# Kernel tuning notes

Hardware: AMD Instinct MI355X
Metric: run time of the kernel (lower is better)

The kernel has to match this reference:

```python
import jax, jax.numpy as jnp
import numpy as np

N_HEADS = 16
DIMS = 1024
HEAD_SIZE = DIMS // N_HEADS


def setup_inputs() -> dict:
    key = jax.random.key(0)
    k1, k2, k3, k4, k5 = jax.random.split(key, 5)
    x = jax.random.normal(k1, (1, 4096, DIMS), dtype=jnp.float32)
    s = 1.0 / np.sqrt(DIMS)
    w_qkv = jax.random.uniform(k2, (3 * DIMS, DIMS), jnp.float32, -s, s)
    b_qkv = jax.random.uniform(k3, (3 * DIMS,), jnp.float32, -s, s)
    w_o = jax.random.uniform(k4, (DIMS, DIMS), jnp.float32, -s, s)
    b_o = jax.random.uniform(k5, (DIMS,), jnp.float32, -s, s)
    return {"x": x, "w_qkv": w_qkv, "b_qkv": b_qkv, "w_o": w_o, "b_o": b_o,
            "causal_mask": 1}


def reference(x, w_qkv, b_qkv, w_o, b_o, causal_mask):
    B, S, D = x.shape
    qkv = x @ w_qkv.T + b_qkv                      # [B,S,3D]
    q, k, v = jnp.split(qkv, 3, axis=-1)
    def heads(t):
        return t.reshape(B, S, N_HEADS, HEAD_SIZE).transpose(0, 2, 1, 3)  # [B,H,S,hd]
    q, k, v = heads(q), heads(k), heads(v)
    scores = jnp.einsum("bhsd,bhtd->bhst", q, k)   # [B,H,S,S]
    if causal_mask:
        tri = jnp.triu(jnp.ones((S, S), dtype=bool), k=1)
        scores = jnp.where(tri, -jnp.inf, scores)  # mask BEFORE scale, as in torch code
    scores = scores / np.sqrt(HEAD_SIZE)
    weights = jax.nn.softmax(scores, axis=-1)
    out = jnp.einsum("bhst,bhtd->bhsd", weights, v)  # [B,H,S,hd]
    out = out.transpose(0, 2, 1, 3).reshape(B, S, D)
    return out @ w_o.T + b_o
```

## Files before the change

### kernel.cpp

```cpp
#include <hip/hip_runtime.h>
#include <hip/hip_bf16.h>
#include <stdint.h>

typedef __attribute__((ext_vector_type(8))) short short8;
typedef __attribute__((ext_vector_type(4))) float f32x4;
typedef __attribute__((ext_vector_type(16))) float f32x16;
typedef __attribute__((ext_vector_type(2))) unsigned int uint2u;
typedef __hip_bfloat16 bf16;

#define S_LEN 4096
#define DMODEL 1024
#define NH 16
#define HD 64
#define QSCALE 0.1803368801111f

static __device__ inline uint2 pack4(float4 v) {
  union { uint2 u; bf16 h[4]; } p;
  p.h[0] = (bf16)v.x; p.h[1] = (bf16)v.y; p.h[2] = (bf16)v.z; p.h[3] = (bf16)v.w;
  return p.u;
}

static __device__ inline uint32_t pack2(float a, float b) {
  union { uint32_t u; bf16 h[2]; } p;
  p.h[0] = (bf16)a; p.h[1] = (bf16)b;
  return p.u;
}

static __device__ inline void gload_lds16(const bf16* g, bf16* l) {
  __builtin_amdgcn_global_load_lds(
      (const __attribute__((address_space(1))) unsigned int*)g,
      (__attribute__((address_space(3))) unsigned int*)l, 16, 0, 0);
}

static __device__ inline int rot_idx(int r, int c) {
  return r * 64 + ((c + ((r & 7) << 3)) & 63);
}

__global__ __launch_bounds__(256)
void cvt_all(const float* __restrict__ x, const float* __restrict__ wq,
             const float* __restrict__ wo, bf16* __restrict__ xb,
             bf16* __restrict__ wqb, bf16* __restrict__ wob) {
  const int nx = S_LEN * DMODEL;
  const int nq = 3 * DMODEL * DMODEL;
  const int no = DMODEL * DMODEL;
  int i = (blockIdx.x * 256 + threadIdx.x) * 4;
  if (i < nx) {
    *(uint2*)(xb + i) = pack4(*(const float4*)(x + i));
  } else if (i < nx + nq) {
    int j = i - nx;
    *(uint2*)(wqb + j) = pack4(*(const float4*)(wq + j));
  } else if (i < nx + nq + no) {
    int j = i - nx - nq;
    *(uint2*)(wob + j) = pack4(*(const float4*)(wo + j));
  }
}

__global__ __launch_bounds__(256)
void gemm_qkv(const bf16* __restrict__ A, const bf16* __restrict__ B,
              const float* __restrict__ bias, bf16* __restrict__ qkv2,
              bf16* __restrict__ vt) {
  const int K = DMODEL;
  __shared__ bf16 sA[128 * 64];
  __shared__ bf16 sB[128 * 64];
  const int tid  = threadIdx.x;
  const int lane = tid & 63;
  const int wave = tid >> 6;
  const int wm = wave >> 1, wn = wave & 1;
  const int tileM = blockIdx.y * 128;
  const int tileN = blockIdx.x * 128;

  const int lrow = lane & 15;
  const int quad = lane >> 4;
  const int kq   = quad * 8;

  f32x4 acc[4][4];
#pragma unroll
  for (int i = 0; i < 4; i++)
#pragma unroll
    for (int j = 0; j < 4; j++) acc[i][j] = (f32x4){0.f, 0.f, 0.f, 0.f};

  const int trl = lane >> 3;
  const int cgl = (((lane & 7) - trl) & 7) << 3;
  const bf16* aP[4];
  const bf16* bP[4];
#pragma unroll
  for (int c = 0; c < 4; c++) {
    int ch = wave * 4 + c;
    aP[c] = A + (size_t)(tileM + ch * 8 + trl) * K + cgl;
    bP[c] = B + (size_t)(tileN + ch * 8 + trl) * K + cgl;
  }

  for (int k0 = 0; k0 < K; k0 += 64) {
    __syncthreads();
#pragma unroll
    for (int c = 0; c < 4; c++) {
      int ch = wave * 4 + c;
      gload_lds16(aP[c] + k0, sA + ch * 512);
      gload_lds16(bP[c] + k0, sB + ch * 512);
    }
    __syncthreads();
#pragma unroll
    for (int ks = 0; ks < 2; ks++) {
      short8 afrag[4], bfrag[4];
#pragma unroll
      for (int mi = 0; mi < 4; mi++)
        afrag[mi] = *(const short8*)(sA + rot_idx(wm * 64 + mi * 16 + lrow, ks * 32 + kq));
#pragma unroll
      for (int ni = 0; ni < 4; ni++)
        bfrag[ni] = *(const short8*)(sB + rot_idx(wn * 64 + ni * 16 + lrow, ks * 32 + kq));
#pragma unroll
      for (int mi = 0; mi < 4; mi++)
#pragma unroll
        for (int ni = 0; ni < 4; ni++)
          acc[mi][ni] = __builtin_amdgcn_mfma_f32_16x16x32_bf16(afrag[mi], bfrag[ni], acc[mi][ni], 0, 0, 0);
    }
  }

#pragma unroll
  for (int ni = 0; ni < 4; ni++) {
    int col = tileN + wn * 64 + ni * 16 + lrow;
    float bv = bias[col];
    if (col < 2 * DMODEL) {
      float sc = (col < DMODEL) ? QSCALE : 1.0f;
#pragma unroll
      for (int mi = 0; mi < 4; mi++) {
        int row0 = tileM + wm * 64 + mi * 16 + quad * 4;
#pragma unroll
        for (int r = 0; r < 4; r++)
          qkv2[(size_t)(row0 + r) * 2048 + col] = (bf16)((acc[mi][ni][r] + bv) * sc);
      }
    } else {
      int cc = col - 2 * DMODEL;
      int hh = cc >> 6, dd = cc & 63;
      bf16* vrow = vt + ((size_t)(hh * 64 + dd)) * S_LEN;
#pragma unroll
      for (int mi = 0; mi < 4; mi++) {
        int row0 = tileM + wm * 64 + mi * 16 + quad * 4;
        float4 v = {acc[mi][ni][0] + bv, acc[mi][ni][1] + bv,
                    acc[mi][ni][2] + bv, acc[mi][ni][3] + bv};
        *(uint2*)(vrow + row0) = pack4(v);
      }
    }
  }
}

__global__ __launch_bounds__(256)
void gemm_oproj(const bf16* __restrict__ A, const bf16* __restrict__ B,
                const float* __restrict__ bias, float* __restrict__ C) {
  const int K = DMODEL, N = DMODEL;
  __shared__ bf16 sA[128 * 64];
  __shared__ bf16 sB[64 * 64];
  const int tid  = threadIdx.x;
  const int lane = tid & 63;
  const int wave = tid >> 6;
  const int wm = wave >> 1, wn = wave & 1;
  const int tileM = blockIdx.y * 128;
  const int tileN = blockIdx.x * 64;

  const int lrow = lane & 15;
  const int quad = lane >> 4;
  const int kq   = quad * 8;

  f32x4 acc[4][2];
#pragma unroll
  for (int i = 0; i < 4; i++)
#pragma unroll
    for (int j = 0; j < 2; j++) acc[i][j] = (f32x4){0.f, 0.f, 0.f, 0.f};

  const int trl = lane >> 3;
  const int cgl = (((lane & 7) - trl) & 7) << 3;
  const bf16* aP[4];
  const bf16* bP[2];
#pragma unroll
  for (int c = 0; c < 4; c++) {
    int ch = wave * 4 + c;
    aP[c] = A + (size_t)(tileM + ch * 8 + trl) * K + cgl;
  }
#pragma unroll
  for (int c = 0; c < 2; c++) {
    int ch = wave * 2 + c;
    bP[c] = B + (size_t)(tileN + ch * 8 + trl) * K + cgl;
  }

  for (int k0 = 0; k0 < K; k0 += 64) {
    __syncthreads();
#pragma unroll
    for (int c = 0; c < 4; c++)
      gload_lds16(aP[c] + k0, sA + (wave * 4 + c) * 512);
#pragma unroll
    for (int c = 0; c < 2; c++)
      gload_lds16(bP[c] + k0, sB + (wave * 2 + c) * 512);
    __syncthreads();
#pragma unroll
    for (int ks = 0; ks < 2; ks++) {
      short8 afrag[4], bfrag[2];
#pragma unroll
      for (int mi = 0; mi < 4; mi++)
        afrag[mi] = *(const short8*)(sA + rot_idx(wm * 64 + mi * 16 + lrow, ks * 32 + kq));
#pragma unroll
      for (int ni = 0; ni < 2; ni++)
        bfrag[ni] = *(const short8*)(sB + rot_idx(wn * 32 + ni * 16 + lrow, ks * 32 + kq));
#pragma unroll
      for (int mi = 0; mi < 4; mi++)
#pragma unroll
        for (int ni = 0; ni < 2; ni++)
          acc[mi][ni] = __builtin_amdgcn_mfma_f32_16x16x32_bf16(afrag[mi], bfrag[ni], acc[mi][ni], 0, 0, 0);
    }
  }

#pragma unroll
  for (int ni = 0; ni < 2; ni++) {
    int col = tileN + wn * 32 + ni * 16 + lrow;
    float bv = bias[col];
#pragma unroll
    for (int mi = 0; mi < 4; mi++) {
      int row0 = tileM + wm * 64 + mi * 16 + quad * 4;
#pragma unroll
      for (int r = 0; r < 4; r++)
        C[(size_t)(row0 + r) * N + col] = acc[mi][ni][r] + bv;
    }
  }
}

__global__ __launch_bounds__(256)
void gemm_qkv_f32(const float* __restrict__ A, const float* __restrict__ B,
                  const float* __restrict__ bias, bf16* __restrict__ qkv2,
                  bf16* __restrict__ vt) {
  const int K = DMODEL;
  __shared__ bf16 sA[128 * 64];
  __shared__ bf16 sB[128 * 64];
  const int tid  = threadIdx.x;
  const int lane = tid & 63;
  const int wave = tid >> 6;
  const int wm = wave >> 1, wn = wave & 1;
  const int tileM = blockIdx.y * 128;
  const int tileN = blockIdx.x * 128;
  const int lrow = lane & 15;
  const int quad = lane >> 4;
  const int kq   = quad * 8;

  f32x4 acc[4][4];
#pragma unroll
  for (int i = 0; i < 4; i++)
#pragma unroll
    for (int j = 0; j < 4; j++) acc[i][j] = (f32x4){0.f, 0.f, 0.f, 0.f};

  const int r0 = tid >> 4;
  const int cc = (tid & 15) * 4;

  for (int k0 = 0; k0 < K; k0 += 64) {
    uint2 ra[8], rb[8];
#pragma unroll
    for (int i = 0; i < 8; i++) {
      int row = r0 + i * 16;
      ra[i] = pack4(*(const float4*)(A + (size_t)(tileM + row) * K + k0 + cc));
      rb[i] = pack4(*(const float4*)(B + (size_t)(tileN + row) * K + k0 + cc));
    }
    __syncthreads();
#pragma unroll
    for (int i = 0; i < 8; i++) {
      int row = r0 + i * 16;
      *(uint2*)(sA + row * 64 + cc) = ra[i];
      *(uint2*)(sB + row * 64 + cc) = rb[i];
    }
    __syncthreads();
#pragma unroll
    for (int ks = 0; ks < 2; ks++) {
      short8 afrag[4], bfrag[4];
#pragma unroll
      for (int mi = 0; mi < 4; mi++)
        afrag[mi] = *(const short8*)(sA + (wm * 64 + mi * 16 + lrow) * 64 + ks * 32 + kq);
#pragma unroll
      for (int ni = 0; ni < 4; ni++)
        bfrag[ni] = *(const short8*)(sB + (wn * 64 + ni * 16 + lrow) * 64 + ks * 32 + kq);
#pragma unroll
      for (int mi = 0; mi < 4; mi++)
#pragma unroll
        for (int ni = 0; ni < 4; ni++)
          acc[mi][ni] = __builtin_amdgcn_mfma_f32_16x16x32_bf16(afrag[mi], bfrag[ni], acc[mi][ni], 0, 0, 0);
    }
  }
#pragma unroll
  for (int ni = 0; ni < 4; ni++) {
    int col = tileN + wn * 64 + ni * 16 + lrow;
    float bv = bias[col];
    if (col < 2 * DMODEL) {
      float sc = (col < DMODEL) ? QSCALE : 1.0f;
#pragma unroll
      for (int mi = 0; mi < 4; mi++) {
        int row0 = tileM + wm * 64 + mi * 16 + quad * 4;
#pragma unroll
        for (int r = 0; r < 4; r++)
          qkv2[(size_t)(row0 + r) * 2048 + col] = (bf16)((acc[mi][ni][r] + bv) * sc);
      }
    } else {
      int c2 = col - 2 * DMODEL;
      int hh = c2 >> 6, dd = c2 & 63;
      bf16* vrow = vt + ((size_t)(hh * 64 + dd)) * S_LEN;
#pragma unroll
      for (int mi = 0; mi < 4; mi++) {
        int row0 = tileM + wm * 64 + mi * 16 + quad * 4;
        float4 v = {acc[mi][ni][0] + bv, acc[mi][ni][1] + bv,
                    acc[mi][ni][2] + bv, acc[mi][ni][3] + bv};
        *(uint2*)(vrow + row0) = pack4(v);
      }
    }
  }
}

__global__ __launch_bounds__(256)
void gemm_oproj_f32w(const bf16* __restrict__ A, const float* __restrict__ B,
                     const float* __restrict__ bias, float* __restrict__ C) {
  const int K = DMODEL, N = DMODEL;
  __shared__ bf16 sA[128 * 64];
  __shared__ bf16 sB[128 * 64];
  const int tid  = threadIdx.x;
  const int lane = tid & 63;
  const int wave = tid >> 6;
  const int wm = wave >> 1, wn = wave & 1;
  const int tileM = blockIdx.y * 128;
  const int tileN = blockIdx.x * 128;
  const int lrow = lane & 15;
  const int quad = lane >> 4;
  const int kq   = quad * 8;

  f32x4 acc[4][4];
#pragma unroll
  for (int i = 0; i < 4; i++)
#pragma unroll
    for (int j = 0; j < 4; j++) acc[i][j] = (f32x4){0.f, 0.f, 0.f, 0.f};

  const int a_r0 = tid >> 3;
  const int a_cc = (tid & 7) * 8;
  const int b_r0 = tid >> 4;
  const int b_cc = (tid & 15) * 4;

  for (int k0 = 0; k0 < K; k0 += 64) {
    uint4 ra[4];
    uint2 rb[8];
#pragma unroll
    for (int i = 0; i < 4; i++)
      ra[i] = *(const uint4*)(A + (size_t)(tileM + a_r0 + i * 32) * K + k0 + a_cc);
#pragma unroll
    for (int i = 0; i < 8; i++)
      rb[i] = pack4(*(const float4*)(B + (size_t)(tileN + b_r0 + i * 16) * K + k0 + b_cc));
    __syncthreads();
#pragma unroll
    for (int i = 0; i < 4; i++)
      *(uint4*)(sA + (a_r0 + i * 32) * 64 + a_cc) = ra[i];
#pragma unroll
    for (int i = 0; i < 8; i++)
      *(uint2*)(sB + (b_r0 + i * 16) * 64 + b_cc) = rb[i];
    __syncthreads();
#pragma unroll
    for (int ks = 0; ks < 2; ks++) {
      short8 afrag[4], bfrag[4];
#pragma unroll
      for (int mi = 0; mi < 4; mi++)
        afrag[mi] = *(const short8*)(sA + (wm * 64 + mi * 16 + lrow) * 64 + ks * 32 + kq);
#pragma unroll
      for (int ni = 0; ni < 4; ni++)
        bfrag[ni] = *(const short8*)(sB + (wn * 64 + ni * 16 + lrow) * 64 + ks * 32 + kq);
#pragma unroll
      for (int mi = 0; mi < 4; mi++)
#pragma unroll
        for (int ni = 0; ni < 4; ni++)
          acc[mi][ni] = __builtin_amdgcn_mfma_f32_16x16x32_bf16(afrag[mi], bfrag[ni], acc[mi][ni], 0, 0, 0);
    }
  }
#pragma unroll
  for (int ni = 0; ni < 4; ni++) {
    int col = tileN + wn * 64 + ni * 16 + lrow;
    float bv = bias[col];
#pragma unroll
    for (int mi = 0; mi < 4; mi++) {
      int row0 = tileM + wm * 64 + mi * 16 + quad * 4;
#pragma unroll
      for (int r = 0; r < 4; r++)
        C[(size_t)(row0 + r) * N + col] = acc[mi][ni][r] + bv;
    }
  }
}

__global__ __launch_bounds__(256, 4)
void attn_kernel(const bf16* __restrict__ qkv2, const bf16* __restrict__ vt,
                 bf16* __restrict__ attn_out, const int* __restrict__ causal_ptr) {
  __shared__ bf16 sQ[64 * 64];
  __shared__ bf16 sK[2][64 * 64];
  __shared__ bf16 sV[2][64 * 64];

  const int tid  = threadIdx.x;
  const int lane = tid & 63;
  const int wave = tid >> 6;
  const int qh   = wave >> 1;
  const int kh   = wave & 1;

  const int id  = blockIdx.y * 64 + blockIdx.x;
  const int xcd = id & 7;
  const int jj  = id >> 3;
  const int hh  = jj >> 6;
  const int h   = xcd + (hh << 3);
  const int qw  = jj & 63;
  const int qi  = hh ? (63 - qw) : qw;
  const int qbase = qi * 64;
  const bool causal = (*causal_ptr) != 0;

  const int l31 = lane & 31;
  const int hi  = lane >> 5;

  const int trl = lane >> 3;
  const int cgl = (((lane & 7) - trl) & 7) << 3;

  const bf16* Qb = qkv2 + h * HD;
  const bf16* Kb = qkv2 + DMODEL + h * HD;
  const bf16* Vb = vt + (size_t)(h * HD) * S_LEN;

#pragma unroll
  for (int i = 0; i < 2; i++) {
    int ch = wave * 2 + i;
    gload_lds16(Qb + (size_t)(qbase + ch * 8 + trl) * 2048 + cgl, sQ + ch * 512);
  }
#pragma unroll
  for (int i = 0; i < 2; i++) {
    int ch = wave * 2 + i;
    int trow = ch * 8 + trl;
    gload_lds16(Kb + (size_t)trow * 2048 + cgl, sK[0] + ch * 512);
    gload_lds16(Vb + (size_t)trow * S_LEN + cgl, sV[0] + ch * 512);
  }

  f32x16 oacc[2];
#pragma unroll
  for (int nc = 0; nc < 2; nc++)
#pragma unroll
    for (int e = 0; e < 16; e++) oacc[nc][e] = 0.f;
  float l_st = 0.f;

  const int nkt = causal ? (qi + 1) : (S_LEN / 64);
  const int wrmin = qbase + qh * 32;
  const int wrmax = wrmin + 31;
  const int q_g   = wrmin + l31;

  __syncthreads();
  short8 qf[4];
#pragma unroll
  for (int kd = 0; kd < 4; kd++)
    qf[kd] = *(const short8*)(sQ + rot_idx(qh * 32 + l31, kd * 16 + hi * 8));

  for (int jt = 0; jt < nkt; jt++) {
    const int cur = jt & 1;
    const int kbase = jt * 64;
    __syncthreads();

    if (jt + 1 < nkt) {
      const int kb2 = kbase + 64;
#pragma unroll
      for (int i = 0; i < 2; i++) {
        int ch = wave * 2 + i;
        int trow = ch * 8 + trl;
        gload_lds16(Kb + (size_t)(kb2 + trow) * 2048 + cgl, sK[cur ^ 1] + ch * 512);
        gload_lds16(Vb + (size_t)trow * S_LEN + kb2 + cgl, sV[cur ^ 1] + ch * 512);
      }
    }
    const int kh32 = kbase + kh * 32;
    if (causal && kh32 > wrmax) continue;

    uint32_t pw[2][4];
    {
      f32x16 sacc;
#pragma unroll
      for (int e = 0; e < 16; e++) sacc[e] = 0.f;
      __builtin_amdgcn_s_setprio(1);
#pragma unroll
      for (int kd = 0; kd < 4; kd++) {
        short8 kf = *(const short8*)(sK[cur] + rot_idx(kh * 32 + l31, kd * 16 + hi * 8));
        sacc = __builtin_amdgcn_mfma_f32_32x32x16_bf16(kf, qf[kd], sacc, 0, 0, 0);
      }
      __builtin_amdgcn_s_setprio(0);
      const bool nm = causal && (kh32 + 31 > wrmin);
      float p[16];
      float psum = 0.f;
#pragma unroll
      for (int g = 0; g < 4; g++) {
#pragma unroll
        for (int r = 0; r < 4; r++) {
          float v = __builtin_amdgcn_exp2f(sacc[g * 4 + r]);
          if (nm) {
            int kg = kh32 + g * 8 + hi * 4 + r;
            if (kg > q_g) v = 0.f;
          }
          p[g * 4 + r] = v;
          psum += v;
        }
      }
      l_st += psum;
      uint32_t pku[4][2];
#pragma unroll
      for (int g = 0; g < 4; g++) {
#pragma unroll
        for (int h2 = 0; h2 < 2; h2++)
          pku[g][h2] = pack2(p[g * 4 + h2 * 2], p[g * 4 + h2 * 2 + 1]);
      }
#pragma unroll
      for (int c2 = 0; c2 < 2; c2++) {
#pragma unroll
        for (int h2 = 0; h2 < 2; h2++) {
          uint2u sw = __builtin_amdgcn_permlane32_swap(
              pku[2 * c2][h2], pku[2 * c2 + 1][h2], false, false);
          pw[c2][h2]     = sw[0];
          pw[c2][2 + h2] = sw[1];
        }
      }
    }

    __builtin_amdgcn_s_setprio(1);
#pragma unroll
    for (int c2 = 0; c2 < 2; c2++) {
      if (causal && (kh32 + c2 * 16 > wrmax)) continue;
      union { short8 s; uint32_t u[4]; } pf;
#pragma unroll
      for (int w = 0; w < 4; w++) pf.u[w] = pw[c2][w];
#pragma unroll
      for (int nc = 0; nc < 2; nc++) {
        short8 vf = *(const short8*)(sV[cur] +
            rot_idx(nc * 32 + l31, (kh * 2 + c2) * 16 + hi * 8));
        oacc[nc] = __builtin_amdgcn_mfma_f32_32x32x16_bf16(pf.s, vf, oacc[nc], 0, 0, 0);
      }
    }
    __builtin_amdgcn_s_setprio(0);
  }

  __syncthreads();
  float ltot = l_st + __shfl_xor(l_st, 32);
  float* obuf = (float*)sK;
  float* lbuf = (float*)sV;
  if (kh == 1) {
    float* ob = obuf + qh * 2048;
#pragma unroll
    for (int nc = 0; nc < 2; nc++)
#pragma unroll
      for (int e = 0; e < 16; e++)
        ob[(nc * 16 + e) * 64 + lane] = oacc[nc][e];
    if (hi == 0) lbuf[qh * 32 + l31] = ltot;
  }
  __syncthreads();
  if (kh == 0) {
    float* ob = obuf + qh * 2048;
#pragma unroll
    for (int nc = 0; nc < 2; nc++)
#pragma unroll
      for (int e = 0; e < 16; e++)
        oacc[nc][e] += ob[(nc * 16 + e) * 64 + lane];
    ltot += lbuf[qh * 32 + l31];
    if (hi == 0) lbuf[64 + qh * 32 + l31] = ltot;
    float invl[4][4];
#pragma unroll
    for (int g = 0; g < 4; g++) {
      f32x4 lv = *(const f32x4*)(lbuf + 64 + qh * 32 + g * 8 + hi * 4);
#pragma unroll
      for (int r = 0; r < 4; r++) invl[g][r] = 1.0f / fmaxf(lv[r], 1e-30f);
    }
#pragma unroll
    for (int nc = 0; nc < 2; nc++) {
#pragma unroll
      for (int g = 0; g < 4; g++) {
#pragma unroll
        for (int r = 0; r < 4; r++) {
          int qg = qbase + qh * 32 + g * 8 + hi * 4 + r;
          int col = h * HD + nc * 32 + l31;
          attn_out[(size_t)qg * DMODEL + col] = (bf16)(oacc[nc][g * 4 + r] * invl[g][r]);
        }
      }
    }
  }
}

extern "C" void kernel_launch(void* const* d_in, const int* in_sizes, int n_in,
                              void* d_out, int out_size, void* d_ws, size_t ws_size,
                              hipStream_t stream) {
  const float* x     = (const float*)d_in[0];
  const float* w_qkv = (const float*)d_in[1];
  const float* b_qkv = (const float*)d_in[2];
  const float* w_o   = (const float*)d_in[3];
  const float* b_o   = (const float*)d_in[4];
  const int*   cm    = (const int*)d_in[5];

  char* ws = (char*)d_ws;
  bf16* qkv2 = (bf16*)ws;
  bf16* vt   = (bf16*)(ws + 16777216);
  bf16* attn = (bf16*)(ws + 25165824);
  bf16* xb   = (bf16*)(ws + 33554432);
  bf16* wqb  = (bf16*)(ws + 41943040);
  bf16* wob  = (bf16*)(ws + 48234496);

  dim3 blk(256);
  const bool fast = (ws_size >= (size_t)50331648);

  if (fast) {
    const int ntot = S_LEN * DMODEL + 3 * DMODEL * DMODEL + DMODEL * DMODEL;
    cvt_all<<<dim3((ntot / 4 + 255) / 256), blk, 0, stream>>>(
        x, w_qkv, w_o, xb, wqb, wob);
    gemm_qkv<<<dim3(3 * DMODEL / 128, S_LEN / 128), blk, 0, stream>>>(
        xb, wqb, b_qkv, qkv2, vt);
    attn_kernel<<<dim3(S_LEN / 64, NH), blk, 0, stream>>>(qkv2, vt, attn, cm);
    gemm_oproj<<<dim3(DMODEL / 64, S_LEN / 128), blk, 0, stream>>>(
        attn, wob, b_o, (float*)d_out);
  } else {
    gemm_qkv_f32<<<dim3(3 * DMODEL / 128, S_LEN / 128), blk, 0, stream>>>(
        x, w_qkv, b_qkv, qkv2, vt);
    attn_kernel<<<dim3(S_LEN / 64, NH), blk, 0, stream>>>(qkv2, vt, attn, cm);
    gemm_oproj_f32w<<<dim3(DMODEL / 128, S_LEN / 128), blk, 0, stream>>>(
        attn, w_o, b_o, (float*)d_out);
  }
}
```

Before: 221.0 us.

## Shrink attention LDS to two tiles to double occupancy

```diff
diff --git a/kernel.cpp b/kernel.cpp
--- a/kernel.cpp
+++ b/kernel.cpp
@@ -382,12 +382,11 @@
   }
 }
 
-__global__ __launch_bounds__(256, 4)
+__global__ __launch_bounds__(256, 8)
 void attn_kernel(const bf16* __restrict__ qkv2, const bf16* __restrict__ vt,
                  bf16* __restrict__ attn_out, const int* __restrict__ causal_ptr) {
-  __shared__ bf16 sQ[64 * 64];
-  __shared__ bf16 sK[2][64 * 64];
-  __shared__ bf16 sV[2][64 * 64];
+  __shared__ bf16 smem[2][64 * 64];
+  __shared__ float lbuf[128];
 
   const int tid  = threadIdx.x;
   const int lane = tid & 63;
@@ -415,64 +414,49 @@
   const bf16* Kb = qkv2 + DMODEL + h * HD;
   const bf16* Vb = vt + (size_t)(h * HD) * S_LEN;
 
-#pragma unroll
-  for (int i = 0; i < 2; i++) {
-    int ch = wave * 2 + i;
-    gload_lds16(Qb + (size_t)(qbase + ch * 8 + trl) * 2048 + cgl, sQ + ch * 512);
-  }
-#pragma unroll
-  for (int i = 0; i < 2; i++) {
-    int ch = wave * 2 + i;
-    int trow = ch * 8 + trl;
-    gload_lds16(Kb + (size_t)trow * 2048 + cgl, sK[0] + ch * 512);
-    gload_lds16(Vb + (size_t)trow * S_LEN + cgl, sV[0] + ch * 512);
-  }
-
-  f32x16 oacc[2];
-#pragma unroll
-  for (int nc = 0; nc < 2; nc++)
-#pragma unroll
-    for (int e = 0; e < 16; e++) oacc[nc][e] = 0.f;
-  float l_st = 0.f;
+  bf16* const A = smem[0];
+  bf16* const B = smem[1];
 
   const int nkt = causal ? (qi + 1) : (S_LEN / 64);
   const int wrmin = qbase + qh * 32;
   const int wrmax = wrmin + 31;
   const int q_g   = wrmin + l31;
 
+#pragma unroll
+  for (int i = 0; i < 2; i++) {
+    int ch = wave * 2 + i;
+    int trow = ch * 8 + trl;
+    gload_lds16(Kb + (size_t)trow * 2048 + cgl, A + ch * 512);
+    gload_lds16(Vb + (size_t)trow * S_LEN + cgl, B + ch * 512);
+  }
+  short8 qf[4];
+#pragma unroll
+  for (int kd = 0; kd < 4; kd++)
+    qf[kd] = *(const short8*)(Qb + (size_t)q_g * 2048 + kd * 16 + hi * 8);
+
+  f32x16 oacc[2];
+#pragma unroll
+  for (int nc = 0; nc < 2; nc++)
+#pragma unroll
+    for (int e = 0; e < 16; e++) oacc[nc][e] = 0.f;
+  float l_st = 0.f;
+
   __syncthreads();
-  short8 qf[4];
-#pragma unroll
-  for (int kd = 0; kd < 4; kd++)
-    qf[kd] = *(const short8*)(sQ + rot_idx(qh * 32 + l31, kd * 16 + hi * 8));
 
   for (int jt = 0; jt < nkt; jt++) {
-    const int cur = jt & 1;
     const int kbase = jt * 64;
-    __syncthreads();
-
-    if (jt + 1 < nkt) {
-      const int kb2 = kbase + 64;
-#pragma unroll
-      for (int i = 0; i < 2; i++) {
-        int ch = wave * 2 + i;
-        int trow = ch * 8 + trl;
-        gload_lds16(Kb + (size_t)(kb2 + trow) * 2048 + cgl, sK[cur ^ 1] + ch * 512);
-        gload_lds16(Vb + (size_t)trow * S_LEN + kb2 + cgl, sV[cur ^ 1] + ch * 512);
-      }
-    }
     const int kh32 = kbase + kh * 32;
-    if (causal && kh32 > wrmax) continue;
+    const bool live = !(causal && kh32 > wrmax);
 
     uint32_t pw[2][4];
-    {
+    if (live) {
       f32x16 sacc;
 #pragma unroll
       for (int e = 0; e < 16; e++) sacc[e] = 0.f;
       __builtin_amdgcn_s_setprio(1);
 #pragma unroll
       for (int kd = 0; kd < 4; kd++) {
-        short8 kf = *(const short8*)(sK[cur] + rot_idx(kh * 32 + l31, kd * 16 + hi * 8));
+        short8 kf = *(const short8*)(A + rot_idx(kh * 32 + l31, kd * 16 + hi * 8));
         sacc = __builtin_amdgcn_mfma_f32_32x32x16_bf16(kf, qf[kd], sacc, 0, 0, 0);
       }
       __builtin_amdgcn_s_setprio(0);
@@ -512,27 +496,51 @@
       }
     }
 
-    __builtin_amdgcn_s_setprio(1);
-#pragma unroll
-    for (int c2 = 0; c2 < 2; c2++) {
-      if (causal && (kh32 + c2 * 16 > wrmax)) continue;
-      union { short8 s; uint32_t u[4]; } pf;
-#pragma unroll
-      for (int w = 0; w < 4; w++) pf.u[w] = pw[c2][w];
-#pragma unroll
-      for (int nc = 0; nc < 2; nc++) {
-        short8 vf = *(const short8*)(sV[cur] +
-            rot_idx(nc * 32 + l31, (kh * 2 + c2) * 16 + hi * 8));
-        oacc[nc] = __builtin_amdgcn_mfma_f32_32x32x16_bf16(pf.s, vf, oacc[nc], 0, 0, 0);
-      }
-    }
-    __builtin_amdgcn_s_setprio(0);
-  }
-
-  __syncthreads();
+    __syncthreads();
+
+    if (jt + 1 < nkt) {
+      const int kb2 = kbase + 64;
+#pragma unroll
+      for (int i = 0; i < 2; i++) {
+        int ch = wave * 2 + i;
+        int trow = ch * 8 + trl;
+        gload_lds16(Kb + (size_t)(kb2 + trow) * 2048 + cgl, A + ch * 512);
+      }
+    }
+
+    if (live) {
+      __builtin_amdgcn_s_setprio(1);
+#pragma unroll
+      for (int c2 = 0; c2 < 2; c2++) {
+        if (causal && (kh32 + c2 * 16 > wrmax)) continue;
+        union { short8 s; uint32_t u[4]; } pf;
+#pragma unroll
+        for (int w = 0; w < 4; w++) pf.u[w] = pw[c2][w];
+#pragma unroll
+        for (int nc = 0; nc < 2; nc++) {
+          short8 vf = *(const short8*)(B +
+              rot_idx(nc * 32 + l31, (kh * 2 + c2) * 16 + hi * 8));
+          oacc[nc] = __builtin_amdgcn_mfma_f32_32x32x16_bf16(pf.s, vf, oacc[nc], 0, 0, 0);
+        }
+      }
+      __builtin_amdgcn_s_setprio(0);
+    }
+
+    __syncthreads();
+
+    if (jt + 1 < nkt) {
+      const int kb2 = kbase + 64;
+#pragma unroll
+      for (int i = 0; i < 2; i++) {
+        int ch = wave * 2 + i;
+        int trow = ch * 8 + trl;
+        gload_lds16(Vb + (size_t)trow * S_LEN + kb2 + cgl, B + ch * 512);
+      }
+    }
+  }
+
   float ltot = l_st + __shfl_xor(l_st, 32);
-  float* obuf = (float*)sK;
-  float* lbuf = (float*)sV;
+  float* obuf = (float*)smem;
   if (kh == 1) {
     float* ob = obuf + qh * 2048;
 #pragma unroll
```

Result: slower. 480.4 us (+117.4%).
